# Optimization experiments

Hardware: AMD Instinct MI355X
Metric: run time of the kernel (lower is better)

The kernel has to match this reference:

```python
import jax, jax.numpy as jnp
import numpy as np
from jax import lax

T, B, D_IN, H, D_OUT = 512, 64, 256, 512, 256


def _lstm_scan(xs, h0, c0, Wih, Whh, b):
    """Standard LSTM over time. xs: [T,B,Din]; returns (hs [T,B,H], hT, cT).
    Gate order i,f,g,o (PyTorch convention)."""
    def step(carry, x_t):
        h, c = carry
        gates = x_t @ Wih.T + h @ Whh.T + b            # [B, 4H]
        i, f, g, o = jnp.split(gates, 4, axis=-1)
        i = jax.nn.sigmoid(i)
        f = jax.nn.sigmoid(f)
        g = jnp.tanh(g)
        o = jax.nn.sigmoid(o)
        c = f * c + i * g
        h = o * jnp.tanh(c)
        return (h, c), h
    (hT, cT), hs = lax.scan(step, (h0, c0), xs)
    return hs, hT, cT


def setup_inputs() -> dict:
    key = jax.random.key(0)
    ks = jax.random.split(key, 10)
    s = 0.05
    return {
        "x": jax.random.normal(ks[0], (T, B, D_IN), jnp.float32),
        "target": jax.random.uniform(ks[1], (T, B, D_OUT), jnp.float32),
        "hidden_state": jnp.zeros((1, B, H), jnp.float32),
        "cell_state": jnp.zeros((1, B, H), jnp.float32),
        "enc_Wih": jax.random.normal(ks[2], (4 * H, D_IN), jnp.float32) * s,
        "enc_Whh": jax.random.normal(ks[3], (4 * H, H), jnp.float32) * s,
        "enc_b": jax.random.normal(ks[4], (4 * H,), jnp.float32) * s,
        "dec_Wih": jax.random.normal(ks[5], (4 * H, D_OUT), jnp.float32) * s,
        "dec_Whh": jax.random.normal(ks[6], (4 * H, H), jnp.float32) * s,
        "dec_b": jax.random.normal(ks[7], (4 * H,), jnp.float32) * s,
        "fc_W": jax.random.normal(ks[8], (D_OUT, H), jnp.float32) * s,
        "fc_b": jax.random.normal(ks[9], (D_OUT,), jnp.float32) * s,
    }


def reference(x, target, hidden_state, cell_state,
              enc_Wih, enc_Whh, enc_b, dec_Wih, dec_Whh, dec_b, fc_W, fc_b):
    # Encoder: consume x, keep final (h, c).
    _, h, c = _lstm_scan(x, hidden_state[0], cell_state[0], enc_Wih, enc_Whh, enc_b)
    # Decoder with teacher_forcing = 1.0: input at step t is target[t-1],
    # step 0 input is zeros (matches torch code's initial x = zeros).
    dec_in = jnp.concatenate([jnp.zeros((1,) + target.shape[1:], target.dtype),
                              target[:-1]], axis=0)          # [T, B, D_OUT]
    hs, _, _ = _lstm_scan(dec_in, h, c, dec_Wih, dec_Whh, dec_b)  # [T, B, H]
    logits = hs @ fc_W.T + fc_b                                   # [T, B, D_OUT]
    return jax.nn.softmax(logits, axis=-1)
```

## Files before the change

kernel.cpp:

```cpp
#include <hip/hip_runtime.h>
#include <math.h>

#define TT 512
#define BB 64
#define DIN 256
#define HH 512
#define DOUT 256

#define RSU 388
#define RSH 776
#define PST 68

#define A_HI_OFF 0
#define A_LO_OFF 6208
#define P_OFF    12416
#define B_OFF    14592
#define C_OFF    14656
#define SMEM_U32 14912
#define SMEM_BYTES (SMEM_U32*4)

#define FCS 516

typedef _Float16 f16x8 __attribute__((ext_vector_type(8)));
typedef float    f32x4 __attribute__((ext_vector_type(4)));
typedef unsigned u32x4 __attribute__((ext_vector_type(4)));

union H16 { _Float16 f; unsigned short u; };
__device__ __forceinline__ unsigned short f16bits(_Float16 h) { H16 t; t.f = h; return t.u; }

__device__ __forceinline__ void pack2(float x, float y, unsigned& hi, unsigned& lo) {
    _Float16 hx = (_Float16)x, hy = (_Float16)y;
    _Float16 lx = (_Float16)((x - (float)hx) * 2048.0f);
    _Float16 ly = (_Float16)((y - (float)hy) * 2048.0f);
    hi = (unsigned)f16bits(hx) | ((unsigned)f16bits(hy) << 16);
    lo = (unsigned)f16bits(lx) | ((unsigned)f16bits(ly) << 16);
}

__device__ __forceinline__ u32x4 ld16_cohere(const void* p) {
    u32x4 v;
    asm volatile("global_load_dwordx4 %0, %1, off sc0 sc1"
                 : "=&v"(v) : "v"(p) : "memory");
    return v;
}
__device__ __forceinline__ void st16_cohere(void* p, u32x4 v) {
    asm volatile("global_store_dwordx4 %0, %1, off sc0 sc1"
                 :: "v"(p), "v"(v) : "memory");
}

__device__ __forceinline__ bool tag_ok(u32x4 v, unsigned par) {
    unsigned a = v[0] & v[1] & v[2] & v[3];
    unsigned o = v[0] | v[1] | v[2] | v[3];
    unsigned x = par ? ~a : o;
    return (x & 0x00010001u) == 0u;
}

__device__ __forceinline__ void load_w_regs(const float* __restrict__ Whh,
                                            const float* __restrict__ Wih,
                                            int u0, int ct, int kh, int m, int q,
                                            f16x8 (&whi)[12], f16x8 (&wlo)[12]) {
    const int C = ct*HH + u0 + m;
    const float* rowH = Whh + (size_t)C*HH;
    const float* rowI = Wih + (size_t)C*DIN;
    #pragma unroll
    for (int jj = 0; jj < 12; ++jj) {
        const int ks = (jj < 8) ? (kh*8 + jj) : (16 + kh*4 + (jj - 8));
        const float* src = (ks < 16) ? (rowH + ks*32 + q*8)
                                     : (rowI + (ks - 16)*32 + q*8);
        float4 a = ((const float4*)src)[0];
        float4 b = ((const float4*)src)[1];
        f16x8 h8, l8; _Float16 t16;
        t16=(_Float16)a.x; h8[0]=t16; l8[0]=(_Float16)((a.x-(float)t16)*2048.0f);
        t16=(_Float16)a.y; h8[1]=t16; l8[1]=(_Float16)((a.y-(float)t16)*2048.0f);
        t16=(_Float16)a.z; h8[2]=t16; l8[2]=(_Float16)((a.z-(float)t16)*2048.0f);
        t16=(_Float16)a.w; h8[3]=t16; l8[3]=(_Float16)((a.w-(float)t16)*2048.0f);
        t16=(_Float16)b.x; h8[4]=t16; l8[4]=(_Float16)((b.x-(float)t16)*2048.0f);
        t16=(_Float16)b.y; h8[5]=t16; l8[5]=(_Float16)((b.y-(float)t16)*2048.0f);
        t16=(_Float16)b.z; h8[6]=t16; l8[6]=(_Float16)((b.z-(float)t16)*2048.0f);
        t16=(_Float16)b.w; h8[7]=t16; l8[7]=(_Float16)((b.w-(float)t16)*2048.0f);
        whi[jj] = h8; wlo[jj] = l8;
    }
}

__device__ __forceinline__ void stage_x_f16(unsigned* __restrict__ sm32,
                                            const float* __restrict__ src, int tid) {
    for (int r = 0; r < 2; ++r) {
        int idx4 = tid + 512*r;
        int b = idx4 >> 6, j4 = idx4 & 63;
        float4 v = ((const float4*)(src + (size_t)b*DIN))[j4];
        unsigned h0, l0, h1, l1;
        pack2(v.x, v.y, h0, l0);
        pack2(v.z, v.w, h1, l1);
        int o = b*RSU + 256 + 2*j4;
        sm32[A_HI_OFF + o]     = h0;
        sm32[A_HI_OFF + o + 1] = h1;
        sm32[A_LO_OFF + o]     = l0;
        sm32[A_LO_OFF + o + 1] = l1;
    }
}

__device__ __forceinline__ void stage_x_zero_f16(unsigned* __restrict__ sm32, int tid) {
    for (int r = 0; r < 2; ++r) {
        int idx = tid + 512*r;
        int row = idx >> 6, j = idx & 63;
        int o = row*RSU + 256 + 2*j;
        sm32[A_HI_OFF + o]     = 0u;
        sm32[A_HI_OFF + o + 1] = 0u;
        sm32[A_LO_OFF + o]     = 0u;
        sm32[A_LO_OFF + o + 1] = 0u;
    }
}

__global__ __launch_bounds__(512, 1)
void lstm_persist(const float* __restrict__ x, const float* __restrict__ target,
                  const float* __restrict__ h0, const float* __restrict__ c0,
                  const float* __restrict__ eWih, const float* __restrict__ eWhh,
                  const float* __restrict__ eb,
                  const float* __restrict__ dWih, const float* __restrict__ dWhh,
                  const float* __restrict__ db,
                  float* __restrict__ hs,
                  unsigned short* __restrict__ hbh,
                  unsigned short* __restrict__ hbl)
{
    extern __shared__ unsigned sm32[];
    float* p_l = (float*)(sm32 + P_OFF);
    float* b_l = (float*)(sm32 + B_OFF);
    float* c_l = (float*)(sm32 + C_OFF);

    const int tid = (int)threadIdx.x;
    const int g   = (int)(blockIdx.x & 3);
    const int ij  = (int)(blockIdx.x >> 2);
    const int b0  = g * 16;
    const int u0  = ij * 16;

    if (tid < 256) {
        int b = tid >> 4, u = tid & 15;
        c_l[tid] = c0[(size_t)(b0 + b)*HH + u0 + u];
    }
    if (tid < 64) b_l[tid] = eb[(tid >> 4)*HH + u0 + (tid & 15)];
    stage_x_f16(sm32, x + (size_t)b0*DIN, tid);
    for (int r = 0; r < 4; ++r) {
        int idx4 = tid + 512*r;
        int b = idx4 >> 7, j4 = idx4 & 127;
        float4 v = ((const float4*)(h0 + (size_t)(b0 + b)*HH))[j4];
        unsigned h0p, l0p, h1p, l1p;
        pack2(v.x, v.y, h0p, l0p);
        pack2(v.z, v.w, h1p, l1p);
        int o = b*RSU + 2*j4;
        sm32[A_HI_OFF + o]     = h0p;
        sm32[A_HI_OFF + o + 1] = h1p;
        sm32[A_LO_OFF + o]     = l0p;
        sm32[A_LO_OFF + o + 1] = l1p;
    }
    __syncthreads();

    const int lane = tid & 63;
    const int wid  = tid >> 6;
    const int m    = lane & 15;
    const int q    = lane >> 4;
    const int ct   = wid & 3;
    const int kh   = wid >> 2;

    const _Float16* aH = (const _Float16*)(sm32 + A_HI_OFF);
    const _Float16* aL = (const _Float16*)(sm32 + A_LO_OFF);
    const int abase = m*RSH + q*8;

    f16x8 whi[12], wlo[12];
    load_w_regs(eWhh, eWih, u0, ct, kh, m, q, whi, wlo);

    for (int s = 0; s < 1024; ++s) {
        f32x4 hh = {0.f,0.f,0.f,0.f}, hl = {0.f,0.f,0.f,0.f}, lh = {0.f,0.f,0.f,0.f};
        #pragma unroll
        for (int jj = 8; jj < 12; ++jj) {
            const int ks = 16 + kh*4 + (jj - 8);
            f16x8 ah = *(const f16x8*)(aH + abase + ks*32);
            f16x8 al = *(const f16x8*)(aL + abase + ks*32);
            hh = __builtin_amdgcn_mfma_f32_16x16x32_f16(ah, whi[jj], hh, 0, 0, 0);
            hl = __builtin_amdgcn_mfma_f32_16x16x32_f16(ah, wlo[jj], hl, 0, 0, 0);
            lh = __builtin_amdgcn_mfma_f32_16x16x32_f16(al, whi[jj], lh, 0, 0, 0);
        }

        if (s > 0) {
            const int slot = s & 1;
            const unsigned par2 = (unsigned)((s >> 1) & 1);
            const u32x4* SH = (const u32x4*)(hbh + (size_t)slot*BB*HH + (size_t)b0*HH);
            const u32x4* SL = (const u32x4*)(hbl + (size_t)slot*BB*HH + (size_t)b0*HH);
            u32x4 v0 = {0,0,0,0}, v1 = {0,0,0,0}, v2 = {0,0,0,0}, v3 = {0,0,0,0};
            unsigned pend = 0xFu;
            do {
                if (pend & 1u) v0 = ld16_cohere(SH + tid);
                if (pend & 2u) v1 = ld16_cohere(SH + tid + 512);
                if (pend & 4u) v2 = ld16_cohere(SL + tid);
                if (pend & 8u) v3 = ld16_cohere(SL + tid + 512);
                asm volatile("s_waitcnt vmcnt(0)"
                             : "+v"(v0), "+v"(v1), "+v"(v2), "+v"(v3) :: "memory");
                if (tag_ok(v0, par2)) pend &= ~1u;
                if (tag_ok(v1, par2)) pend &= ~2u;
                if (tag_ok(v2, par2)) pend &= ~4u;
                if (tag_ok(v3, par2)) pend &= ~8u;
            } while (pend);
            const int j = tid & 63, r0 = tid >> 6;
            *(u32x4*)(sm32 + A_HI_OFF + (r0    )*RSU + j*4) = v0;
            *(u32x4*)(sm32 + A_HI_OFF + (r0 + 8)*RSU + j*4) = v1;
            *(u32x4*)(sm32 + A_LO_OFF + (r0    )*RSU + j*4) = v2;
            *(u32x4*)(sm32 + A_LO_OFF + (r0 + 8)*RSU + j*4) = v3;
            __syncthreads();
        }

        #pragma unroll
        for (int jj = 0; jj < 8; ++jj) {
            const int ks = kh*8 + jj;
            f16x8 ah = *(const f16x8*)(aH + abase + ks*32);
            f16x8 al = *(const f16x8*)(aL + abase + ks*32);
            hh = __builtin_amdgcn_mfma_f32_16x16x32_f16(ah, whi[jj], hh, 0, 0, 0);
            hl = __builtin_amdgcn_mfma_f32_16x16x32_f16(ah, wlo[jj], hl, 0, 0, 0);
            lh = __builtin_amdgcn_mfma_f32_16x16x32_f16(al, whi[jj], lh, 0, 0, 0);
        }
        {
            const float sc = 1.0f/2048.0f;
            float* pb = p_l + (kh*16 + q*4)*PST + ct*16 + m;
            #pragma unroll
            for (int i = 0; i < 4; ++i)
                pb[i*PST] = hh[i] + (hl[i] + lh[i])*sc;
        }
        __syncthreads();

        const unsigned par = (unsigned)(((s + 1) >> 1) & 1);

        float hval = 0.f;
        if (tid < 256) {
            const int b = tid >> 4, u = tid & 15;
            const float* p0 = p_l + (size_t)b*PST;
            const float* p1 = p_l + (size_t)(16 + b)*PST;
            float gi = b_l[u]      + p0[u]      + p1[u];
            float gf = b_l[16 + u] + p0[16 + u] + p1[16 + u];
            float gg = b_l[32 + u] + p0[32 + u] + p1[32 + u];
            float go = b_l[48 + u] + p0[48 + u] + p1[48 + u];
            float ii = 1.f/(1.f + expf(-gi));
            float ff = 1.f/(1.f + expf(-gf));
            float g2 = tanhf(gg);
            float oo = 1.f/(1.f + expf(-go));
            float c  = ff*c_l[tid] + ii*g2;
            c_l[tid] = c;
            hval = oo*tanhf(c);
            _Float16 hh16 = (_Float16)hval;
            unsigned uh = ((unsigned)f16bits(hh16) & 0xFFFEu) | par;
            H16 t16; t16.u = (unsigned short)uh;
            _Float16 hl16 = (_Float16)((hval - (float)t16.f) * 2048.0f);
            unsigned ul = ((unsigned)f16bits(hl16) & 0xFFFEu) | par;

            asm volatile("s_waitcnt vmcnt(0)" ::: "memory");
            unsigned r0h = uh | (__shfl_xor(uh, 1, 64) << 16);
            unsigned r0l = ul | (__shfl_xor(ul, 1, 64) << 16);
            u32x4 vh, vl;
            vh[0] = r0h; vh[1] = __shfl_xor(r0h, 2, 64);
            vh[2] = __shfl_xor(r0h, 4, 64); vh[3] = __shfl_xor(r0h, 6, 64);
            vl[0] = r0l; vl[1] = __shfl_xor(r0l, 2, 64);
            vl[2] = __shfl_xor(r0l, 4, 64); vl[3] = __shfl_xor(r0l, 6, 64);
            if ((u & 7) == 0) {
                const int h16 = u >> 3;
                size_t off = (size_t)((s & 1) ^ 1)*BB*HH
                           + (size_t)(b0 + b)*HH + u0 + h16*8;
                st16_cohere(hbh + off, vh);
                st16_cohere(hbl + off, vl);
            }
        }

        if (s >= 512 && tid < 256) {
            int b = tid >> 4, u = tid & 15;
            hs[((size_t)(s - 512)*BB + (b0 + b))*HH + (u0 + u)] = hval;
        }
        if (s == 511) {
            load_w_regs(dWhh, dWih, u0, ct, kh, m, q, whi, wlo);
            if (tid < 64) b_l[tid] = db[(tid >> 4)*HH + u0 + (tid & 15)];
        }
        {
            int ns = s + 1;
            if (ns < 1024) {
                if (ns == 512)       stage_x_zero_f16(sm32, tid);
                else if (ns < 512)   stage_x_f16(sm32, x + ((size_t)ns*BB + b0)*DIN, tid);
                else                 stage_x_f16(sm32, target + ((size_t)(ns - 513)*BB + b0)*DOUT, tid);
            }
        }
        __syncthreads();
    }
}

__global__ __launch_bounds__(256, 1)
void fc_kernel(const float* __restrict__ hs, const float* __restrict__ W,
               const float* __restrict__ bias, float* __restrict__ out)
{
    extern __shared__ float sm[];
    float* hs_l = sm;
    float* w_l  = sm + 16*FCS;

    const int tid = (int)threadIdx.x;
    const int rb = (int)(blockIdx.x >> 3);
    const int cb = (int)(blockIdx.x & 7);

    for (int r = 0; r < 8; ++r) {
        int id = tid + 256*r;
        int b = id >> 7, j = id & 127;
        float4 v = ((const float4*)(hs + (size_t)(rb*16 + b)*HH))[j];
        *(float4*)(hs_l + b*FCS + 4*j) = v;
    }
    for (int r = 0; r < 16; ++r) {
        int id = tid + 256*r;
        int c = id >> 7, j = id & 127;
        float4 v = ((const float4*)(W + (size_t)(cb*32 + c)*HH))[j];
        *(float4*)(w_l + c*FCS + 4*j) = v;
    }
    __syncthreads();

    const int kc = tid & 7, bt = (tid >> 3) & 3, ct = tid >> 5;
    float acc[4][4] = {};
    const float* ap = hs_l + (bt*4)*FCS + 4*kc;
    const float* wp = w_l  + (ct*4)*FCS + 4*kc;
    #pragma unroll 4
    for (int i = 0; i < 16; ++i) {
        float4 av[4], wv[4];
        #pragma unroll
        for (int q = 0; q < 4; ++q) av[q] = *(const float4*)(ap + q*FCS + 32*i);
        #pragma unroll
        for (int q = 0; q < 4; ++q) wv[q] = *(const float4*)(wp + q*FCS + 32*i);
        #pragma unroll
        for (int b2 = 0; b2 < 4; ++b2)
            #pragma unroll
            for (int c2 = 0; c2 < 4; ++c2)
                acc[b2][c2] += av[b2].x*wv[c2].x + av[b2].y*wv[c2].y
                             + av[b2].z*wv[c2].z + av[b2].w*wv[c2].w;
    }
    #pragma unroll
    for (int b2 = 0; b2 < 4; ++b2)
        #pragma unroll
        for (int c2 = 0; c2 < 4; ++c2) {
            float v = acc[b2][c2];
            v += __shfl_xor(v, 1, 64);
            v += __shfl_xor(v, 2, 64);
            v += __shfl_xor(v, 4, 64);
            acc[b2][c2] = v;
        }
    if (kc == 0) {
        #pragma unroll
        for (int b2 = 0; b2 < 4; ++b2)
            #pragma unroll
            for (int c2 = 0; c2 < 4; ++c2) {
                int row = rb*16 + bt*4 + b2;
                int col = cb*32 + ct*4 + c2;
                out[(size_t)row*DOUT + col] = acc[b2][c2] + bias[col];
            }
    }
}

__global__ __launch_bounds__(256, 1)
void softmax_kernel(float* __restrict__ out)
{
    int row  = (int)blockIdx.x * 4 + ((int)threadIdx.x >> 6);
    int lane = (int)threadIdx.x & 63;
    float4 v = ((const float4*)(out + (size_t)row*DOUT))[lane];
    float m = fmaxf(fmaxf(v.x, v.y), fmaxf(v.z, v.w));
    #pragma unroll
    for (int d = 1; d < 64; d <<= 1) m = fmaxf(m, __shfl_xor(m, d, 64));
    float ex = expf(v.x - m), ey = expf(v.y - m), ez = expf(v.z - m), ew = expf(v.w - m);
    float ssum = ex + ey + ez + ew;
    #pragma unroll
    for (int d = 1; d < 64; d <<= 1) ssum += __shfl_xor(ssum, d, 64);
    float inv = 1.f / ssum;
    float4 o = make_float4(ex*inv, ey*inv, ez*inv, ew*inv);
    ((float4*)(out + (size_t)row*DOUT))[lane] = o;
}

__global__ void init_kernel(unsigned* __restrict__ hbh32, unsigned* __restrict__ hbl32)
{
    int i = (int)blockIdx.x * 256 + (int)threadIdx.x;
    unsigned* base = (i < 8192) ? hbh32 : hbl32;
    int j = (i & 8191) * 4;
    unsigned val = (j < 16384) ? 0u : 0x00010001u;
    u32x4 v = {val, val, val, val};
    st16_cohere(base + j, v);
}

extern "C" void kernel_launch(void* const* d_in, const int* in_sizes, int n_in,
                              void* d_out, int out_size, void* d_ws, size_t ws_size,
                              hipStream_t stream) {
    (void)in_sizes; (void)n_in; (void)out_size; (void)ws_size;
    const float* x      = (const float*)d_in[0];
    const float* target = (const float*)d_in[1];
    const float* h0     = (const float*)d_in[2];
    const float* c0     = (const float*)d_in[3];
    const float* eWih   = (const float*)d_in[4];
    const float* eWhh   = (const float*)d_in[5];
    const float* eb     = (const float*)d_in[6];
    const float* dWih   = (const float*)d_in[7];
    const float* dWhh   = (const float*)d_in[8];
    const float* db     = (const float*)d_in[9];
    const float* fcW    = (const float*)d_in[10];
    const float* fcb    = (const float*)d_in[11];
    float* out = (float*)d_out;

    float* hs = (float*)d_ws + 1024;
    unsigned short* hbh = (unsigned short*)(hs + (size_t)TT*BB*HH);
    unsigned short* hbl = hbh + (size_t)2*BB*HH;

    init_kernel<<<dim3(64), dim3(256), 0, stream>>>((unsigned*)hbh, (unsigned*)hbl);

    lstm_persist<<<dim3(128), dim3(512), SMEM_BYTES, stream>>>(
        x, target, h0, c0, eWih, eWhh, eb, dWih, dWhh, db, hs, hbh, hbl);

    size_t lds_fc = (size_t)(48*FCS) * sizeof(float);
    fc_kernel<<<dim3(16384), dim3(256), lds_fc, stream>>>(hs, fcW, fcb, out);

    softmax_kernel<<<dim3(8192), dim3(256), 0, stream>>>(out);
}
```

Before: 4.173 ms.

## Split each block's 16 batch rows into two 8-row halves pipelined per step

Result: slower. 4.745 ms (+13.7%).

```diff
diff --git a/kernel.cpp b/kernel.cpp
--- a/kernel.cpp
+++ b/kernel.cpp
@@ -81,33 +81,57 @@
     }
 }
 
-__device__ __forceinline__ void stage_x_f16(unsigned* __restrict__ sm32,
-                                            const float* __restrict__ src, int tid) {
+__device__ __forceinline__ void stage_x8(unsigned* __restrict__ sm32,
+                                         const float* __restrict__ src,
+                                         int row0, int t, int srcstride) {
     for (int r = 0; r < 2; ++r) {
-        int idx4 = tid + 512*r;
+        int idx4 = t + 256*r;
         int b = idx4 >> 6, j4 = idx4 & 63;
-        float4 v = ((const float4*)(src + (size_t)b*DIN))[j4];
+        float4 v = ((const float4*)(src + (size_t)b*srcstride))[j4];
         unsigned h0, l0, h1, l1;
         pack2(v.x, v.y, h0, l0);
         pack2(v.z, v.w, h1, l1);
-        int o = b*RSU + 256 + 2*j4;
+        int o = (row0 + b)*RSU + 256 + 2*j4;
         sm32[A_HI_OFF + o]     = h0;
         sm32[A_HI_OFF + o + 1] = h1;
         sm32[A_LO_OFF + o]     = l0;
         sm32[A_LO_OFF + o + 1] = l1;
     }
 }
-
-__device__ __forceinline__ void stage_x_zero_f16(unsigned* __restrict__ sm32, int tid) {
+__device__ __forceinline__ void stage_x8_zero(unsigned* __restrict__ sm32,
+                                              int row0, int t) {
     for (int r = 0; r < 2; ++r) {
-        int idx = tid + 512*r;
-        int row = idx >> 6, j = idx & 63;
-        int o = row*RSU + 256 + 2*j;
+        int idx = t + 256*r;
+        int b = idx >> 6, j = idx & 63;
+        int o = (row0 + b)*RSU + 256 + 2*j;
         sm32[A_HI_OFF + o]     = 0u;
         sm32[A_HI_OFF + o + 1] = 0u;
         sm32[A_LO_OFF + o]     = 0u;
         sm32[A_LO_OFF + o + 1] = 0u;
     }
+}
+
+__device__ __forceinline__ void gather8(unsigned* __restrict__ sm32,
+                                        const unsigned short* __restrict__ hbh,
+                                        const unsigned short* __restrict__ hbl,
+                                        int slot, unsigned par, int gbase,
+                                        int row0, int tid) {
+    const unsigned short* SH = hbh + (size_t)slot*BB*HH + (size_t)gbase*HH;
+    const unsigned short* SL = hbl + (size_t)slot*BB*HH + (size_t)gbase*HH;
+    const int b = tid >> 6, j = tid & 63;
+    const void* ph = SH + (size_t)b*HH + j*8;
+    const void* pl = SL + (size_t)b*HH + j*8;
+    u32x4 vh = {0,0,0,0}, vl = {0,0,0,0};
+    unsigned pend = 3u;
+    do {
+        if (pend & 1u) vh = ld16_cohere(ph);
+        if (pend & 2u) vl = ld16_cohere(pl);
+        asm volatile("s_waitcnt vmcnt(0)" : "+v"(vh), "+v"(vl) :: "memory");
+        if (tag_ok(vh, par)) pend &= ~1u;
+        if (tag_ok(vl, par)) pend &= ~2u;
+    } while (pend);
+    *(u32x4*)(sm32 + A_HI_OFF + (row0 + b)*RSU + j*4) = vh;
+    *(u32x4*)(sm32 + A_LO_OFF + (row0 + b)*RSU + j*4) = vl;
 }
 
 __global__ __launch_bounds__(512, 1)
@@ -126,30 +150,48 @@
     float* b_l = (float*)(sm32 + B_OFF);
     float* c_l = (float*)(sm32 + C_OFF);
 
-    const int tid = (int)threadIdx.x;
-    const int g   = (int)(blockIdx.x & 3);
-    const int ij  = (int)(blockIdx.x >> 2);
-    const int b0  = g * 16;
-    const int u0  = ij * 16;
+    const int tid   = (int)threadIdx.x;
+    const int pair  = (int)(blockIdx.x & 3);
+    const int ij    = (int)(blockIdx.x >> 2);
+    const int baseA = pair * 16;
+    const int baseB = baseA + 8;
+    const int u0    = ij * 16;
 
     if (tid < 256) {
-        int b = tid >> 4, u = tid & 15;
-        c_l[tid] = c0[(size_t)(b0 + b)*HH + u0 + u];
+        int loc = tid & 127, b = loc >> 4, u = loc & 15;
+        int batch = (tid < 128 ? baseA : baseB) + b;
+        c_l[tid] = c0[(size_t)batch*HH + u0 + u];
     }
     if (tid < 64) b_l[tid] = eb[(tid >> 4)*HH + u0 + (tid & 15)];
-    stage_x_f16(sm32, x + (size_t)b0*DIN, tid);
     for (int r = 0; r < 4; ++r) {
         int idx4 = tid + 512*r;
-        int b = idx4 >> 7, j4 = idx4 & 127;
-        float4 v = ((const float4*)(h0 + (size_t)(b0 + b)*HH))[j4];
+        int row = idx4 >> 7, j4 = idx4 & 127;
+        int batch = (row < 8) ? (baseA + row) : (baseB + row - 8);
+        float4 v = ((const float4*)(h0 + (size_t)batch*HH))[j4];
         unsigned h0p, l0p, h1p, l1p;
         pack2(v.x, v.y, h0p, l0p);
         pack2(v.z, v.w, h1p, l1p);
-        int o = b*RSU + 2*j4;
+        int o = row*RSU + 2*j4;
         sm32[A_HI_OFF + o]     = h0p;
         sm32[A_HI_OFF + o + 1] = h1p;
         sm32[A_LO_OFF + o]     = l0p;
         sm32[A_LO_OFF + o + 1] = l1p;
+    }
+    {
+        for (int r = 0; r < 2; ++r) {
+            int idx4 = tid + 512*r;
+            int row = idx4 >> 6, j4 = idx4 & 63;
+            int batch = (row < 8) ? (baseA + row) : (baseB + row - 8);
+            float4 v = ((const float4*)(x + (size_t)batch*DIN))[j4];
+            unsigned h0p, l0p, h1p, l1p;
+            pack2(v.x, v.y, h0p, l0p);
+            pack2(v.z, v.w, h1p, l1p);
+            int o = row*RSU + 256 + 2*j4;
+            sm32[A_HI_OFF + o]     = h0p;
+            sm32[A_HI_OFF + o + 1] = h1p;
+            sm32[A_LO_OFF + o]     = l0p;
+            sm32[A_LO_OFF + o + 1] = l1p;
+        }
     }
     __syncthreads();
 
@@ -167,67 +209,35 @@
     f16x8 whi[12], wlo[12];
     load_w_regs(eWhh, eWih, u0, ct, kh, m, q, whi, wlo);
 
+    const float sc = 1.0f/2048.0f;
+
     for (int s = 0; s < 1024; ++s) {
-        f32x4 hh = {0.f,0.f,0.f,0.f}, hl = {0.f,0.f,0.f,0.f}, lh = {0.f,0.f,0.f,0.f};
-        #pragma unroll
-        for (int jj = 8; jj < 12; ++jj) {
-            const int ks = 16 + kh*4 + (jj - 8);
-            f16x8 ah = *(const f16x8*)(aH + abase + ks*32);
-            f16x8 al = *(const f16x8*)(aL + abase + ks*32);
-            hh = __builtin_amdgcn_mfma_f32_16x16x32_f16(ah, whi[jj], hh, 0, 0, 0);
-            hl = __builtin_amdgcn_mfma_f32_16x16x32_f16(ah, wlo[jj], hl, 0, 0, 0);
-            lh = __builtin_amdgcn_mfma_f32_16x16x32_f16(al, whi[jj], lh, 0, 0, 0);
-        }
-
-        if (s > 0) {
-            const int slot = s & 1;
-            const unsigned par2 = (unsigned)((s >> 1) & 1);
-            const u32x4* SH = (const u32x4*)(hbh + (size_t)slot*BB*HH + (size_t)b0*HH);
-            const u32x4* SL = (const u32x4*)(hbl + (size_t)slot*BB*HH + (size_t)b0*HH);
-            u32x4 v0 = {0,0,0,0}, v1 = {0,0,0,0}, v2 = {0,0,0,0}, v3 = {0,0,0,0};
-            unsigned pend = 0xFu;
-            do {
-                if (pend & 1u) v0 = ld16_cohere(SH + tid);
-                if (pend & 2u) v1 = ld16_cohere(SH + tid + 512);
-                if (pend & 4u) v2 = ld16_cohere(SL + tid);
-                if (pend & 8u) v3 = ld16_cohere(SL + tid + 512);
-                asm volatile("s_waitcnt vmcnt(0)"
-                             : "+v"(v0), "+v"(v1), "+v"(v2), "+v"(v3) :: "memory");
-                if (tag_ok(v0, par2)) pend &= ~1u;
-                if (tag_ok(v1, par2)) pend &= ~2u;
-                if (tag_ok(v2, par2)) pend &= ~4u;
-                if (tag_ok(v3, par2)) pend &= ~8u;
-            } while (pend);
-            const int j = tid & 63, r0 = tid >> 6;
-            *(u32x4*)(sm32 + A_HI_OFF + (r0    )*RSU + j*4) = v0;
-            *(u32x4*)(sm32 + A_HI_OFF + (r0 + 8)*RSU + j*4) = v1;
-            *(u32x4*)(sm32 + A_LO_OFF + (r0    )*RSU + j*4) = v2;
-            *(u32x4*)(sm32 + A_LO_OFF + (r0 + 8)*RSU + j*4) = v3;
-            __syncthreads();
-        }
-
-        #pragma unroll
-        for (int jj = 0; jj < 8; ++jj) {
-            const int ks = kh*8 + jj;
-            f16x8 ah = *(const f16x8*)(aH + abase + ks*32);
-            f16x8 al = *(const f16x8*)(aL + abase + ks*32);
-            hh = __builtin_amdgcn_mfma_f32_16x16x32_f16(ah, whi[jj], hh, 0, 0, 0);
-            hl = __builtin_amdgcn_mfma_f32_16x16x32_f16(ah, wlo[jj], hl, 0, 0, 0);
-            lh = __builtin_amdgcn_mfma_f32_16x16x32_f16(al, whi[jj], lh, 0, 0, 0);
-        }
+        const int slotG = s & 1;
+        const unsigned parG = (unsigned)((s >> 1) & 1);
+        const int slotP = (s & 1) ^ 1;
+        const unsigned parP = (unsigned)(((s + 1) >> 1) & 1);
+
+        if (s > 0) gather8(sm32, hbh, hbl, slotG, parG, baseA, 0, tid);
+        __syncthreads();
+
         {
-            const float sc = 1.0f/2048.0f;
+            f32x4 hh = {0.f,0.f,0.f,0.f}, lo = {0.f,0.f,0.f,0.f};
+            #pragma unroll
+            for (int jj = 0; jj < 12; ++jj) {
+                const int ks = (jj < 8) ? (kh*8 + jj) : (16 + kh*4 + (jj - 8));
+                f16x8 ah = *(const f16x8*)(aH + abase + ks*32);
+                f16x8 al = *(const f16x8*)(aL + abase + ks*32);
+                hh = __builtin_amdgcn_mfma_f32_16x16x32_f16(ah, whi[jj], hh, 0, 0, 0);
+                lo = __builtin_amdgcn_mfma_f32_16x16x32_f16(al, whi[jj],
+                     __builtin_amdgcn_mfma_f32_16x16x32_f16(ah, wlo[jj], lo, 0, 0, 0), 0, 0, 0);
+            }
             float* pb = p_l + (kh*16 + q*4)*PST + ct*16 + m;
             #pragma unroll
-            for (int i = 0; i < 4; ++i)
-                pb[i*PST] = hh[i] + (hl[i] + lh[i])*sc;
+            for (int i = 0; i < 4; ++i) pb[i*PST] = hh[i] + lo[i]*sc;
         }
         __syncthreads();
 
-        const unsigned par = (unsigned)(((s + 1) >> 1) & 1);
-
-        float hval = 0.f;
-        if (tid < 256) {
+        if (tid < 128) {
             const int b = tid >> 4, u = tid & 15;
             const float* p0 = p_l + (size_t)b*PST;
             const float* p1 = p_l + (size_t)(16 + b)*PST;
@@ -241,13 +251,14 @@
             float oo = 1.f/(1.f + expf(-go));
             float c  = ff*c_l[tid] + ii*g2;
             c_l[tid] = c;
-            hval = oo*tanhf(c);
+            float hval = oo*tanhf(c);
+            if (s >= 512)
+                hs[((size_t)(s - 512)*BB + (baseA + b))*HH + (u0 + u)] = hval;
             _Float16 hh16 = (_Float16)hval;
-            unsigned uh = ((unsigned)f16bits(hh16) & 0xFFFEu) | par;
+            unsigned uh = ((unsigned)f16bits(hh16) & 0xFFFEu) | parP;
             H16 t16; t16.u = (unsigned short)uh;
             _Float16 hl16 = (_Float16)((hval - (float)t16.f) * 2048.0f);
-            unsigned ul = ((unsigned)f16bits(hl16) & 0xFFFEu) | par;
-
+            unsigned ul = ((unsigned)f16bits(hl16) & 0xFFFEu) | parP;
             asm volatile("s_waitcnt vmcnt(0)" ::: "memory");
             unsigned r0h = uh | (__shfl_xor(uh, 1, 64) << 16);
             unsigned r0l = ul | (__shfl_xor(ul, 1, 64) << 16);
@@ -258,28 +269,83 @@
             vl[2] = __shfl_xor(r0l, 4, 64); vl[3] = __shfl_xor(r0l, 6, 64);
             if ((u & 7) == 0) {
                 const int h16 = u >> 3;
-                size_t off = (size_t)((s & 1) ^ 1)*BB*HH
-                           + (size_t)(b0 + b)*HH + u0 + h16*8;
+                size_t off = (size_t)slotP*BB*HH + (size_t)(baseA + b)*HH + u0 + h16*8;
                 st16_cohere(hbh + off, vh);
                 st16_cohere(hbl + off, vl);
             }
-        }
-
-        if (s >= 512 && tid < 256) {
-            int b = tid >> 4, u = tid & 15;
-            hs[((size_t)(s - 512)*BB + (b0 + b))*HH + (u0 + u)] = hval;
+        } else if (tid >= 256) {
+            int t = tid - 256;
+            if (s < 512)       stage_x8(sm32, x + ((size_t)s*BB + baseB)*DIN, 8, t, DIN);
+            else if (s == 512) stage_x8_zero(sm32, 8, t);
+            else               stage_x8(sm32, target + ((size_t)(s - 513)*BB + baseB)*DOUT, 8, t, DOUT);
+        }
+
+        if (s > 0) gather8(sm32, hbh, hbl, slotG, parG, baseB, 8, tid);
+        __syncthreads();
+
+        {
+            f32x4 hh = {0.f,0.f,0.f,0.f}, lo = {0.f,0.f,0.f,0.f};
+            #pragma unroll
+            for (int jj = 0; jj < 12; ++jj) {
+                const int ks = (jj < 8) ? (kh*8 + jj) : (16 + kh*4 + (jj - 8));
+                f16x8 ah = *(const f16x8*)(aH + abase + ks*32);
+                f16x8 al = *(const f16x8*)(aL + abase + ks*32);
+                hh = __builtin_amdgcn_mfma_f32_16x16x32_f16(ah, whi[jj], hh, 0, 0, 0);
+                lo = __builtin_amdgcn_mfma_f32_16x16x32_f16(al, whi[jj],
+                     __builtin_amdgcn_mfma_f32_16x16x32_f16(ah, wlo[jj], lo, 0, 0, 0), 0, 0, 0);
+            }
+            float* pb = p_l + (kh*16 + q*4)*PST + ct*16 + m;
+            #pragma unroll
+            for (int i = 0; i < 4; ++i) pb[i*PST] = hh[i] + lo[i]*sc;
+        }
+        __syncthreads();
+
+        if (tid >= 128 && tid < 256) {
+            const int t2 = tid - 128;
+            const int b = t2 >> 4, u = t2 & 15;
+            const float* p0 = p_l + (size_t)(8 + b)*PST;
+            const float* p1 = p_l + (size_t)(24 + b)*PST;
+            float gi = b_l[u]      + p0[u]      + p1[u];
+            float gf = b_l[16 + u] + p0[16 + u] + p1[16 + u];
+            float gg = b_l[32 + u] + p0[32 + u] + p1[32 + u];
+            float go = b_l[48 + u] + p0[48 + u] + p1[48 + u];
+            float ii = 1.f/(1.f + expf(-gi));
+            float ff = 1.f/(1.f + expf(-gf));
+            float g2 = tanhf(gg);
+            float oo = 1.f/(1.f + expf(-go));
+            float c  = ff*c_l[tid] + ii*g2;
+            c_l[tid] = c;
+            float hval = oo*tanhf(c);
+            if (s >= 512)
+                hs[((size_t)(s - 512)*BB + (baseB + b))*HH + (u0 + u)] = hval;
+            _Float16 hh16 = (_Float16)hval;
+            unsigned uh = ((unsigned)f16bits(hh16) & 0xFFFEu) | parP;
+            H16 t16; t16.u = (unsigned short)uh;
+            _Float16 hl16 = (_Float16)((hval - (float)t16.f) * 2048.0f);
+            unsigned ul = ((unsigned)f16bits(hl16) & 0xFFFEu) | parP;
+            asm volatile("s_waitcnt vmcnt(0)" ::: "memory");
+            unsigned r0h = uh | (__shfl_xor(uh, 1, 64) << 16);
+            unsigned r0l = ul | (__shfl_xor(ul, 1, 64) << 16);
+            u32x4 vh, vl;
+            vh[0] = r0h; vh[1] = __shfl_xor(r0h, 2, 64);
+            vh[2] = __shfl_xor(r0h, 4, 64); vh[3] = __shfl_xor(r0h, 6, 64);
+            vl[0] = r0l; vl[1] = __shfl_xor(r0l, 2, 64);
+            vl[2] = __shfl_xor(r0l, 4, 64); vl[3] = __shfl_xor(r0l, 6, 64);
+            if ((u & 7) == 0) {
+                const int h16 = u >> 3;
+                size_t off = (size_t)slotP*BB*HH + (size_t)(baseB + b)*HH + u0 + h16*8;
+                st16_cohere(hbh + off, vh);
+                st16_cohere(hbl + off, vl);
+            }
+        } else if (tid >= 256) {
+            int t = tid - 256, ns = s + 1;
+            if (ns < 512)       stage_x8(sm32, x + ((size_t)ns*BB + baseA)*DIN, 0, t, DIN);
+            else if (ns == 512) stage_x8_zero(sm32, 0, t);
+            else if (ns < 1024) stage_x8(sm32, target + ((size_t)(ns - 513)*BB + baseA)*DOUT, 0, t, DOUT);
         }
         if (s == 511) {
             load_w_regs(dWhh, dWih, u0, ct, kh, m, q, whi, wlo);
             if (tid < 64) b_l[tid] = db[(tid >> 4)*HH + u0 + (tid & 15)];
-        }
-        {
-            int ns = s + 1;
-            if (ns < 1024) {
-                if (ns == 512)       stage_x_zero_f16(sm32, tid);
-                else if (ns < 512)   stage_x_f16(sm32, x + ((size_t)ns*BB + b0)*DIN, tid);
-                else                 stage_x_f16(sm32, target + ((size_t)(ns - 513)*BB + b0)*DOUT, tid);
-            }
         }
         __syncthreads();
     }
```
